# Kernel optimization log

Hardware: AMD Instinct MI355X
Metric: run time of the kernel (lower is better)

Reference implementation:

```python
import jax, jax.numpy as jnp
import numpy as np
import math

D = 256   # d_model / hidden_size
Q = 256   # q_num (query-side nodes)
K = 512   # k_num (key-side nodes)
NEG = -9e15


def _forward(q_enc, k_enc, rel_k, rel_v, k_adj,
             W_glob, b_glob, W_gv0, b_gv0, W_gv1, b_gv1,
             W_gq, b_gq, W_lq, b_lq,
             W_locgate, b_locgate, W_gate, b_gate):
    d = q_enc.shape[-1]
    scale = 1.0 / math.sqrt(d)
    act = jnp.tanh  # activation_func='tanh'

    # --- global sigmoid blending of k_enc with the mean query encoding ---
    q_glob_enc = jnp.mean(q_enc, axis=0)                       # [d]
    k_s = jax.nn.sigmoid((q_glob_enc @ W_glob + b_glob) @ k_enc.T * scale)  # [K]
    k_s = k_s[:, None]                                         # [K,1]
    g_1 = q_glob_enc @ W_gv0 + b_gv0                           # [d]
    k_1 = k_enc @ W_gv1 + b_gv1                                # [K,d]
    k_enc2 = (1.0 - k_s) * k_1 + k_s * g_1                     # [K,d]

    # --- global relation-aware attention over k nodes ---
    q_glob = q_enc @ W_gq + b_gq                               # [Q,d]
    qk_logit = q_glob @ k_enc2.T                               # [Q,K]
    qk_r = jnp.einsum('qd,qkd->qk', q_glob, rel_k)             # [Q,K]
    glob_attn = jax.nn.softmax(act((qk_logit + qk_r) * scale), axis=-1)  # [Q,K]

    # --- local adjacency-masked attention ---
    q_loc = q_enc @ W_lq + b_lq                                # [Q,d]
    qnk_logit = q_loc @ k_enc2.T                               # [Q,K]
    qnk_r = jnp.einsum('qd,qkd->qk', q_loc, rel_k)             # [Q,K]
    loc_attn = act((qnk_logit + qnk_r) * scale)                # [Q,K]
    # loc_weight_rep[q,i,j] = loc_attn[q,j]  (repeat + view in torch)
    mask = (k_adj != 0)[None, :, :]                            # [1,K,K]
    masked = jnp.where(mask, loc_attn[:, None, :], NEG)        # [Q,K,K]
    attn_adj_norm = jax.nn.softmax(masked, axis=-1)            # [Q,K,K]
    k_loc = jnp.einsum('qij,jd->qid', attn_adj_norm, k_enc2)   # [Q,K,d]

    # --- local gate between neighborhood value and self value ---
    # sigmoid(cat([k_loc, k_self]) @ W_locgate + b); k_self is broadcast k_enc2
    Wg1, Wg2 = W_locgate[:d], W_locgate[d:]                    # [d,1] each
    gate_logit = (jnp.einsum('qid,d->qi', k_loc, Wg1[:, 0])
                  + (k_enc2 @ Wg2)[None, :, 0] + b_locgate[0])  # [Q,K]
    loc_gate = jax.nn.sigmoid(gate_logit)[..., None]           # [Q,K,1]
    k_awr = loc_gate * k_loc + (1.0 - loc_gate) * k_enc2[None, :, :]  # [Q,K,d]

    # --- aggregate with global attention + relation values ---
    k_matmul = jnp.einsum('qk,qkd->qd', glob_attn, k_awr)      # [Q,d]
    k_r_matmul = jnp.einsum('qk,qkd->qd', glob_attn, rel_v)    # [Q,d]
    q_enc_new = k_matmul + k_r_matmul                          # [Q,d]

    # --- residual gate ---
    Wq1, Wq2 = W_gate[:d], W_gate[d:]
    gate = jax.nn.sigmoid(q_enc_new @ Wq1 + q_enc @ Wq2 + b_gate)  # [Q,1]
    h = gate * q_enc_new + (1.0 - gate) * q_enc                # [Q,d]
    return h


def setup_inputs() -> dict:
    key = jax.random.key(0)
    ks = jax.random.split(key, 16)
    def w(k, shape):
        return jax.random.normal(k, shape, jnp.float32) * 0.02
    return {
        'q_enc': jax.random.normal(ks[0], (Q, D), jnp.float32),
        'k_enc': jax.random.normal(ks[1], (K, D), jnp.float32),
        'rel_k': jax.random.normal(ks[2], (Q, K, D), jnp.float32) * 0.1,
        'rel_v': jax.random.normal(ks[3], (Q, K, D), jnp.float32) * 0.1,
        'k_adj': jax.random.randint(ks[4], (K, K), 0, 2, jnp.int64) if jax.config.jax_enable_x64 else jax.random.randint(ks[4], (K, K), 0, 2, jnp.int32),
        'W_glob': w(ks[5], (D, D)), 'b_glob': jnp.zeros((D,), jnp.float32),
        'W_gv0': w(ks[6], (D, D)), 'b_gv0': jnp.zeros((D,), jnp.float32),
        'W_gv1': w(ks[7], (D, D)), 'b_gv1': jnp.zeros((D,), jnp.float32),
        'W_gq': w(ks[8], (D, D)), 'b_gq': jnp.zeros((D,), jnp.float32),
        'W_lq': w(ks[9], (D, D)), 'b_lq': jnp.zeros((D,), jnp.float32),
        'W_locgate': w(ks[10], (2 * D, 1)), 'b_locgate': jnp.zeros((1,), jnp.float32),
        'W_gate': w(ks[11], (2 * D, 1)), 'b_gate': jnp.zeros((1,), jnp.float32),
    }


def reference(q_enc, k_enc, rel_k, rel_v, k_adj,
              W_glob, b_glob, W_gv0, b_gv0, W_gv1, b_gv1,
              W_gq, b_gq, W_lq, b_lq,
              W_locgate, b_locgate, W_gate, b_gate):
    return _forward(q_enc, k_enc, rel_k, rel_v, k_adj,
                    W_glob, b_glob, W_gv0, b_gv0, W_gv1, b_gv1,
                    W_gq, b_gq, W_lq, b_lq,
                    W_locgate, b_locgate, W_gate, b_gate)
```

## Files before the change

kernel.cpp:

```cpp
#include <hip/hip_runtime.h>
#include <math.h>

#define QN 256
#define KN 512
#define DN 256
#define SCALE 0.0625f

typedef __attribute__((ext_vector_type(8))) short short8v;
typedef __attribute__((ext_vector_type(4))) float f32x4;

__device__ __forceinline__ float sigf(float x){ return 1.0f/(1.0f+expf(-x)); }

__device__ __forceinline__ unsigned short f2bf(float x){
  unsigned u = __float_as_uint(x);
  unsigned r = (u + 0x7FFFu + ((u >> 16) & 1u)) >> 16;
  return (unsigned short)r;
}

__device__ __forceinline__ short8v ld8(const unsigned short* p){
  ushort4 a = *(const ushort4*)p;
  ushort4 b = *(const ushort4*)(p + 16);
  short8v r;
  r[0]=(short)a.x; r[1]=(short)a.y; r[2]=(short)a.z; r[3]=(short)a.w;
  r[4]=(short)b.x; r[5]=(short)b.y; r[6]=(short)b.z; r[7]=(short)b.w;
  return r;
}

__device__ __forceinline__ float wave_red(float v){
  #pragma unroll
  for (int off = 32; off; off >>= 1) v += __shfl_down(v, off);
  return v;
}

__global__ void kA2(const float* __restrict__ q_enc,
                    const float* __restrict__ W_glob, const float* __restrict__ W_gv0,
                    float* __restrict__ party0, float* __restrict__ party1,
                    const int* __restrict__ kadj, unsigned short* __restrict__ mbf){
  __shared__ float sm[256][9];
  __shared__ float qm[8];
  int b = blockIdx.x, t = threadIdx.x;
  int j0 = b*8;
  #pragma unroll
  for (int i = 0; i < 8; ++i){
    int gi = b*2048 + i*256 + t;
    int4 v = ((const int4*)kadj)[gi];
    ushort4 o;
    o.x = v.x ? 0x3F80 : 0; o.y = v.y ? 0x3F80 : 0;
    o.z = v.z ? 0x3F80 : 0; o.w = v.w ? 0x3F80 : 0;
    ((ushort4*)mbf)[gi] = o;
  }
  float4 lo = *(const float4*)(q_enc + (size_t)t*DN + j0);
  float4 hi = *(const float4*)(q_enc + (size_t)t*DN + j0 + 4);
  sm[t][0]=lo.x; sm[t][1]=lo.y; sm[t][2]=lo.z; sm[t][3]=lo.w;
  sm[t][4]=hi.x; sm[t][5]=hi.y; sm[t][6]=hi.z; sm[t][7]=hi.w;
  __syncthreads();
  #pragma unroll
  for (int s = 128; s > 0; s >>= 1){
    if (t < s){
      #pragma unroll
      for (int j = 0; j < 8; ++j) sm[t][j] += sm[t+s][j];
    }
    __syncthreads();
  }
  if (t < 8) qm[t] = sm[0][t] * (1.0f/QN);
  __syncthreads();
  float a0 = 0.f, a1 = 0.f;
  #pragma unroll
  for (int j = 0; j < 8; ++j){
    float s = qm[j];
    a0 = fmaf(s, W_glob[(size_t)(j0+j)*DN + t], a0);
    a1 = fmaf(s, W_gv0[(size_t)(j0+j)*DN + t], a1);
  }
  party0[b*256 + t] = a0; party1[b*256 + t] = a1;
}

__global__ void k23(const float* __restrict__ k_enc,
                    const float* __restrict__ W_gv1, const float* __restrict__ b_gv1,
                    const float* __restrict__ party0, const float* __restrict__ party1,
                    const float* __restrict__ b_glob, const float* __restrict__ b_gv0,
                    const float* __restrict__ W_locgate,
                    float* __restrict__ k_enc2, float* __restrict__ cvec,
                    float* __restrict__ gl2,
                    const float* __restrict__ q_enc,
                    const float* __restrict__ W_gq, const float* __restrict__ b_gq,
                    const float* __restrict__ W_lq, const float* __restrict__ b_lq,
                    float* __restrict__ q_glob, float* __restrict__ q_loc){
  __shared__ float sh1[256];
  __shared__ float red8[8];
  int bid = blockIdx.x, t = threadIdx.x;
  int w = t >> 6, lane = t & 63;
  if (bid < 512){
    int k = bid;
    float tg = b_glob[t], g1v = b_gv0[t];
    #pragma unroll 8
    for (int b2 = 0; b2 < 32; ++b2){
      tg  += party0[b2*256 + t];
      g1v += party1[b2*256 + t];
    }
    float kv = k_enc[(size_t)k*DN + t];
    sh1[t] = kv;
    float part = wave_red(kv * tg);
    if (lane == 0) red8[w] = part;
    __syncthreads();
    float dot = red8[0] + red8[1] + red8[2] + red8[3];
    float ks = sigf(dot * SCALE);
    float acc = b_gv1[t];
    #pragma unroll 8
    for (int j = 0; j < DN; ++j) acc = fmaf(sh1[j], W_gv1[(size_t)j*DN + t], acc);
    float v = (1.f - ks)*acc + ks*g1v;
    k_enc2[(size_t)k*DN + t] = v;
    float pc = wave_red(v * W_locgate[t]);
    float pg = wave_red(v * W_locgate[DN + t]);
    __syncthreads();
    if (lane == 0){ red8[w] = pc; red8[4 + w] = pg; }
    __syncthreads();
    if (t == 0) cvec[k] = red8[0] + red8[1] + red8[2] + red8[3];
    if (t == 1) gl2[k]  = red8[4] + red8[5] + red8[6] + red8[7];
  } else {
    int q = bid - 512;
    sh1[t] = q_enc[(size_t)q*DN + t];
    __syncthreads();
    float a = b_gq[t], b = b_lq[t];
    #pragma unroll 8
    for (int j = 0; j < DN; ++j){
      float s = sh1[j];
      a = fmaf(s, W_gq[(size_t)j*DN + t], a);
      b = fmaf(s, W_lq[(size_t)j*DN + t], b);
    }
    q_glob[(size_t)q*DN + t] = a; q_loc[(size_t)q*DN + t] = b;
  }
}

__global__ __launch_bounds__(256) void kbf(const float* __restrict__ rel_k,
                    const float* __restrict__ rel_v,
                    const float* __restrict__ q_glob, const float* __restrict__ q_loc,
                    const float* __restrict__ ke2, const float* __restrict__ cvec,
                    float* __restrict__ exs,
                    unsigned short* __restrict__ ebf, unsigned short* __restrict__ ecbf,
                    float* __restrict__ part){
  __shared__ f32x4 sacc[4][16][4];
  int t = threadIdx.x;
  int wv = t >> 6, lane = t & 63;
  int g = lane >> 4, l16 = lane & 15;
  int b = blockIdx.x;
  int q = b >> 3, slice = b & 7;
  int base = lane & 48;
  float4 a4[4], b4[4];
  #pragma unroll
  for (int it = 0; it < 4; ++it){
    int d = it*64 + l16*4;
    a4[it] = *(const float4*)(q_glob + (size_t)q*DN + d);
    b4[it] = *(const float4*)(q_loc  + (size_t)q*DN + d);
  }
  f32x4 racc[4];
  #pragma unroll
  for (int it = 0; it < 4; ++it) racc[it] = (f32x4){0.f,0.f,0.f,0.f};

  int k = slice*64 + wv*4 + g;
  size_t ro = ((size_t)q*KN + k)*DN;
  f32x4 x[4], y[4];
  #pragma unroll
  for (int it = 0; it < 4; ++it){
    int d = it*64 + l16*4;
    x[it] = __builtin_nontemporal_load((const f32x4*)(rel_k + ro + d));
    y[it] = __builtin_nontemporal_load((const f32x4*)(rel_v + ro + d));
  }
  #pragma unroll
  for (int kq = 0; kq < 4; ++kq){
    f32x4 xn[4], yn[4];
    if (kq < 3){
      size_t ro2 = ((size_t)q*KN + (k + 16))*DN;
      #pragma unroll
      for (int it = 0; it < 4; ++it){
        int d = it*64 + l16*4;
        xn[it] = __builtin_nontemporal_load((const f32x4*)(rel_k + ro2 + d));
        yn[it] = __builtin_nontemporal_load((const f32x4*)(rel_v + ro2 + d));
      }
    }
    float p1 = 0.f, p2 = 0.f, p3 = 0.f, p4 = 0.f;
    #pragma unroll
    for (int it = 0; it < 4; ++it){
      int d = it*64 + l16*4;
      float4 c = *(const float4*)(ke2 + (size_t)k*DN + d);
      float4 a = a4[it], bb = b4[it];
      p1 += x[it][0]*a.x  + x[it][1]*a.y  + x[it][2]*a.z  + x[it][3]*a.w;
      p2 += x[it][0]*bb.x + x[it][1]*bb.y + x[it][2]*bb.z + x[it][3]*bb.w;
      p3 += c.x*a.x  + c.y*a.y  + c.z*a.z  + c.w*a.w;
      p4 += c.x*bb.x + c.y*bb.y + c.z*bb.z + c.w*bb.w;
    }
    #pragma unroll
    for (int off = 8; off; off >>= 1){
      p1 += __shfl_down(p1, off); p2 += __shfl_down(p2, off);
      p3 += __shfl_down(p3, off); p4 += __shfl_down(p4, off);
    }
    float p13 = __shfl(p1 + p3, base);
    float p24 = __shfl(p2 + p4, base);
    float exv = expf(tanhf(p13*SCALE));
    float evv = expf(tanhf(p24*SCALE));
    if (l16 == 0){
      size_t idx = (size_t)q*KN + k;
      exs[idx] = exv;
      ebf[idx] = f2bf(evv);
      ecbf[idx] = f2bf(evv * cvec[k]);
    }
    #pragma unroll
    for (int it = 0; it < 4; ++it){
      racc[it][0] = fmaf(exv, y[it][0], racc[it][0]);
      racc[it][1] = fmaf(exv, y[it][1], racc[it][1]);
      racc[it][2] = fmaf(exv, y[it][2], racc[it][2]);
      racc[it][3] = fmaf(exv, y[it][3], racc[it][3]);
    }
    if (kq < 3){
      #pragma unroll
      for (int it = 0; it < 4; ++it){ x[it] = xn[it]; y[it] = yn[it]; }
      k += 16;
    }
  }
  #pragma unroll
  for (int h = 16; h <= 32; h <<= 1){
    #pragma unroll
    for (int it = 0; it < 4; ++it){
      racc[it][0] += __shfl_xor(racc[it][0], h);
      racc[it][1] += __shfl_xor(racc[it][1], h);
      racc[it][2] += __shfl_xor(racc[it][2], h);
      racc[it][3] += __shfl_xor(racc[it][3], h);
    }
  }
  if (lane < 16){
    #pragma unroll
    for (int it = 0; it < 4; ++it) sacc[wv][lane][it] = racc[it];
  }
  __syncthreads();
  if (t < 64){
    int it = t >> 4, lb = t & 15;
    f32x4 r0 = sacc[0][lb][it], r1 = sacc[1][lb][it];
    f32x4 r2 = sacc[2][lb][it], r3 = sacc[3][lb][it];
    f32x4 r = r0 + r1 + r2 + r3;
    int d = it*64 + lb*4;
    *(f32x4*)(part + ((size_t)slice*QN + q)*DN + d) = r;
  }
}

__global__ __launch_bounds__(256) void kcA2m(const unsigned short* __restrict__ ebf,
                                             const unsigned short* __restrict__ ecbf,
                                             const unsigned short* __restrict__ mbf,
                                             const float* __restrict__ exs,
                                             const float* __restrict__ gl2,
                                             const float* __restrict__ blg_p,
                                             unsigned short* __restrict__ wvbf,
                                             float* __restrict__ v2){
  __shared__ unsigned short Ae[16*520];
  __shared__ unsigned short Ac[16*520];
  __shared__ unsigned short Bm[64*520];
  int t = threadIdx.x;
  int i0 = blockIdx.x*64, q0 = blockIdx.y*16;
  #pragma unroll
  for (int it = 0; it < 4; ++it){
    int c = t + 256*it; int row = c >> 6, col = (c & 63)*8;
    *(uint4*)&Ae[row*520 + col] = *(const uint4*)&ebf[(size_t)(q0+row)*KN + col];
    *(uint4*)&Ac[row*520 + col] = *(const uint4*)&ecbf[(size_t)(q0+row)*KN + col];
  }
  #pragma unroll
  for (int it = 0; it < 16; ++it){
    int c = t + 256*it; int row = c >> 6, col = (c & 63)*8;
    *(uint4*)&Bm[row*520 + col] = *(const uint4*)&mbf[(size_t)(i0+row)*KN + col];
  }
  __syncthreads();
  int w = t >> 6, l = t & 63;
  int g16 = l >> 4, l16 = l & 15;
  f32x4 aS = {0.f,0.f,0.f,0.f}, aN = {0.f,0.f,0.f,0.f};
  const unsigned short* pe = &Ae[l16*520];
  const unsigned short* pc = &Ac[l16*520];
  const unsigned short* pb = &Bm[(16*w + l16)*520];
  #pragma unroll
  for (int kk = 0; kk < 16; ++kk){
    int k0 = kk*32 + 4*g16;
    short8v fa = ld8(pe + k0);
    short8v fc = ld8(pc + k0);
    short8v fb = ld8(pb + k0);
    aS = __builtin_amdgcn_mfma_f32_16x16x32_bf16(fa, fb, aS, 0, 0, 0);
    aN = __builtin_amdgcn_mfma_f32_16x16x32_bf16(fc, fb, aN, 0, 0, 0);
  }
  float blg = blg_p[0];
  int i = i0 + 16*w + l16;
  float gli = gl2[i];
  #pragma unroll
  for (int r = 0; r < 4; ++r){
    int q = q0 + 4*g16 + r;
    size_t idx = (size_t)q*KN + i;
    float s = aS[r], n = aN[r];
    float lgv = sigf(n/s + gli + blg);
    float ex = exs[idx];
    wvbf[idx] = f2bf(ex*lgv/s);
    v2[idx] = ex*(1.f - lgv);
  }
}

__global__ __launch_bounds__(256) void kcC2m(const unsigned short* __restrict__ wvbf,
                                             const unsigned short* __restrict__ mbf,
                                             const unsigned short* __restrict__ ebf,
                                             const float* __restrict__ v2,
                                             float* __restrict__ coef){
  __shared__ unsigned short Aw[16*520];
  __shared__ unsigned short Bm2[512*72];
  int t = threadIdx.x;
  int j0 = blockIdx.x*64, q0 = blockIdx.y*16;
  #pragma unroll
  for (int it = 0; it < 4; ++it){
    int c = t + 256*it; int row = c >> 6, col = (c & 63)*8;
    *(uint4*)&Aw[row*520 + col] = *(const uint4*)&wvbf[(size_t)(q0+row)*KN + col];
  }
  #pragma unroll
  for (int it = 0; it < 16; ++it){
    int c = t + 256*it; int row = c >> 3, col = (c & 7)*8;
    *(uint4*)&Bm2[row*72 + col] = *(const uint4*)&mbf[(size_t)row*KN + j0 + col];
  }
  __syncthreads();
  int w = t >> 6, l = t & 63;
  int g16 = l >> 4, l16 = l & 15;
  f32x4 aU = {0.f,0.f,0.f,0.f};
  const unsigned short* pa = &Aw[l16*520];
  int nn = 16*w + l16;
  #pragma unroll
  for (int kk = 0; kk < 16; ++kk){
    int k0 = kk*32 + 4*g16;
    short8v fa = ld8(pa + k0);
    short8v fb;
    #pragma unroll
    for (int e = 0; e < 4; ++e){
      fb[e]   = (short)Bm2[(k0+e)*72 + nn];
      fb[4+e] = (short)Bm2[(k0+16+e)*72 + nn];
    }
    aU = __builtin_amdgcn_mfma_f32_16x16x32_bf16(fa, fb, aU, 0, 0, 0);
  }
  int j = j0 + nn;
  #pragma unroll
  for (int r = 0; r < 4; ++r){
    int q = q0 + 4*g16 + r;
    size_t idx = (size_t)q*KN + j;
    float evv = __uint_as_float(((unsigned)ebf[idx]) << 16);
    coef[idx] = aU[r]*evv + v2[idx];
  }
}

__global__ __launch_bounds__(1024) void kE2(const float* __restrict__ ke2,
                                            const float* __restrict__ exs,
                                            const float* __restrict__ coef,
                                            const float* __restrict__ part,
                                            const float* __restrict__ q_enc,
                                            const float* __restrict__ W_gate,
                                            const float* __restrict__ b_gate,
                                            float* __restrict__ out){
  __shared__ float red[512];
  __shared__ float4 pacc[16][64];
  int q = blockIdx.x, t = threadIdx.x, w = t >> 6, lane = t & 63;
  if (t < 512) red[t] = exs[(size_t)q*KN + t];
  __syncthreads();
  #pragma unroll
  for (int s = 256; s > 0; s >>= 1){
    if (t < s) red[t] += red[t+s];
    __syncthreads();
  }
  float invs = 1.0f / red[0];
  float4 acc;
  if ((w & 1) == 0){
    f32x4 pv = *(const f32x4*)(part + ((size_t)(w >> 1)*QN + q)*DN + lane*4);
    acc = make_float4(pv[0], pv[1], pv[2], pv[3]);
  } else {
    acc = make_float4(0.f, 0.f, 0.f, 0.f);
  }
  int kbase = w*32;
  #pragma unroll 8
  for (int kk = 0; kk < 32; ++kk){
    int k = kbase + kk;
    float ck = coef[(size_t)q*KN + k];
    float4 kv = ((const float4*)(ke2 + (size_t)k*DN))[lane];
    acc.x = fmaf(ck, kv.x, acc.x);
    acc.y = fmaf(ck, kv.y, acc.y);
    acc.z = fmaf(ck, kv.z, acc.z);
    acc.w = fmaf(ck, kv.w, acc.w);
  }
  pacc[w][lane] = acc;
  __syncthreads();
  if (t < 64){
    float4 r = pacc[0][t];
    #pragma unroll
    for (int w2 = 1; w2 < 16; ++w2){
      float4 p = pacc[w2][t];
      r.x += p.x; r.y += p.y; r.z += p.z; r.w += p.w;
    }
    r.x *= invs; r.y *= invs; r.z *= invs; r.w *= invs;
    float4 qe = ((const float4*)(q_enc + (size_t)q*DN))[t];
    float4 w1 = ((const float4*)(W_gate))[t];
    float4 w2v = ((const float4*)(W_gate + DN))[t];
    float pd = r.x*w1.x + r.y*w1.y + r.z*w1.z + r.w*w1.w
             + qe.x*w2v.x + qe.y*w2v.y + qe.z*w2v.z + qe.w*w2v.w;
    #pragma unroll
    for (int off = 32; off; off >>= 1) pd += __shfl_down(pd, off);
    float gate = sigf(__shfl(pd, 0) + b_gate[0]);
    float4 h;
    h.x = gate*r.x + (1.f-gate)*qe.x;
    h.y = gate*r.y + (1.f-gate)*qe.y;
    h.z = gate*r.z + (1.f-gate)*qe.z;
    h.w = gate*r.w + (1.f-gate)*qe.w;
    ((float4*)(out + (size_t)q*DN))[t] = h;
  }
}

extern "C" void kernel_launch(void* const* d_in, const int* in_sizes, int n_in,
                              void* d_out, int out_size, void* d_ws, size_t ws_size,
                              hipStream_t stream){
  const float* q_enc     = (const float*)d_in[0];
  const float* k_enc     = (const float*)d_in[1];
  const float* rel_k     = (const float*)d_in[2];
  const float* rel_v     = (const float*)d_in[3];
  const int*   k_adj     = (const int*)  d_in[4];
  const float* W_glob    = (const float*)d_in[5];
  const float* b_glob    = (const float*)d_in[6];
  const float* W_gv0     = (const float*)d_in[7];
  const float* b_gv0     = (const float*)d_in[8];
  const float* W_gv1     = (const float*)d_in[9];
  const float* b_gv1     = (const float*)d_in[10];
  const float* W_gq      = (const float*)d_in[11];
  const float* b_gq      = (const float*)d_in[12];
  const float* W_lq      = (const float*)d_in[13];
  const float* b_lq      = (const float*)d_in[14];
  const float* W_locgate = (const float*)d_in[15];
  const float* b_locgate = (const float*)d_in[16];
  const float* W_gate    = (const float*)d_in[17];
  const float* b_gate    = (const float*)d_in[18];
  float* out = (float*)d_out;

  float* ws = (float*)d_ws;
  float* party0   = ws;
  float* party1   = party0 + 8192;
  float* k_enc2   = party1 + 8192;
  float* cvec     = k_enc2 + 131072;
  float* gl2      = cvec + 512;
  float* q_glob   = gl2 + 512;
  float* q_loc    = q_glob + 65536;
  float* exs      = q_loc + 65536;
  float* v2       = exs + 131072;
  float* coef     = v2 + 131072;
  float* part     = coef + 131072;
  unsigned short* mbf  = (unsigned short*)(part + 524288);
  unsigned short* ebf  = mbf + 262144;
  unsigned short* ecbf = ebf + 131072;
  unsigned short* wvbf = ecbf + 131072;

  kA2<<<32, 256, 0, stream>>>(q_enc, W_glob, W_gv0, party0, party1, k_adj, mbf);
  k23<<<768, 256, 0, stream>>>(k_enc, W_gv1, b_gv1, party0, party1, b_glob, b_gv0,
                               W_locgate, k_enc2, cvec, gl2,
                               q_enc, W_gq, b_gq, W_lq, b_lq, q_glob, q_loc);
  kbf<<<2048, 256, 0, stream>>>(rel_k, rel_v, q_glob, q_loc, k_enc2, cvec,
                                exs, ebf, ecbf, part);
  kcA2m<<<dim3(8, 16), 256, 0, stream>>>(ebf, ecbf, mbf, exs, gl2, b_locgate, wvbf, v2);
  kcC2m<<<dim3(8, 16), 256, 0, stream>>>(wvbf, mbf, ebf, v2, coef);
  kE2<<<256, 1024, 0, stream>>>(k_enc2, exs, coef, part, q_enc, W_gate, b_gate, out);
}
```

Baseline: 88.41 us.

## Fuse masked-coefficient matmul kernel into final output kernel

Removes the separate MFMA kernel that computed coef = (wv @ mask) * e + v2 and folds it into the final per-query kernel. The fused version computes it with scalar FMAs reading the bf16 adjacency matrix directly, and keeps the coefficients in shared memory. This saves one launch and the coef round trip through global memory. In exchange, each of the 256 blocks rereads the full 512x512 bf16 mask (about 512KB per block, mostly from L2) and does the work on scalar ALUs instead of matrix cores.

```diff
diff --git a/kernel.cpp b/kernel.cpp
--- a/kernel.cpp
+++ b/kernel.cpp
@@ -296,65 +296,27 @@
   }
 }
 
-__global__ __launch_bounds__(256) void kcC2m(const unsigned short* __restrict__ wvbf,
-                                             const unsigned short* __restrict__ mbf,
-                                             const unsigned short* __restrict__ ebf,
-                                             const float* __restrict__ v2,
-                                             float* __restrict__ coef){
-  __shared__ unsigned short Aw[16*520];
-  __shared__ unsigned short Bm2[512*72];
-  int t = threadIdx.x;
-  int j0 = blockIdx.x*64, q0 = blockIdx.y*16;
-  #pragma unroll
-  for (int it = 0; it < 4; ++it){
-    int c = t + 256*it; int row = c >> 6, col = (c & 63)*8;
-    *(uint4*)&Aw[row*520 + col] = *(const uint4*)&wvbf[(size_t)(q0+row)*KN + col];
-  }
-  #pragma unroll
-  for (int it = 0; it < 16; ++it){
-    int c = t + 256*it; int row = c >> 3, col = (c & 7)*8;
-    *(uint4*)&Bm2[row*72 + col] = *(const uint4*)&mbf[(size_t)row*KN + j0 + col];
-  }
-  __syncthreads();
-  int w = t >> 6, l = t & 63;
-  int g16 = l >> 4, l16 = l & 15;
-  f32x4 aU = {0.f,0.f,0.f,0.f};
-  const unsigned short* pa = &Aw[l16*520];
-  int nn = 16*w + l16;
-  #pragma unroll
-  for (int kk = 0; kk < 16; ++kk){
-    int k0 = kk*32 + 4*g16;
-    short8v fa = ld8(pa + k0);
-    short8v fb;
-    #pragma unroll
-    for (int e = 0; e < 4; ++e){
-      fb[e]   = (short)Bm2[(k0+e)*72 + nn];
-      fb[4+e] = (short)Bm2[(k0+16+e)*72 + nn];
-    }
-    aU = __builtin_amdgcn_mfma_f32_16x16x32_bf16(fa, fb, aU, 0, 0, 0);
-  }
-  int j = j0 + nn;
-  #pragma unroll
-  for (int r = 0; r < 4; ++r){
-    int q = q0 + 4*g16 + r;
-    size_t idx = (size_t)q*KN + j;
-    float evv = __uint_as_float(((unsigned)ebf[idx]) << 16);
-    coef[idx] = aU[r]*evv + v2[idx];
-  }
-}
-
-__global__ __launch_bounds__(1024) void kE2(const float* __restrict__ ke2,
+__global__ __launch_bounds__(1024) void kE3(const float* __restrict__ ke2,
                                             const float* __restrict__ exs,
-                                            const float* __restrict__ coef,
+                                            const unsigned short* __restrict__ wvbf,
+                                            const unsigned short* __restrict__ mbf,
+                                            const unsigned short* __restrict__ ebf,
+                                            const float* __restrict__ v2,
                                             const float* __restrict__ part,
                                             const float* __restrict__ q_enc,
                                             const float* __restrict__ W_gate,
                                             const float* __restrict__ b_gate,
                                             float* __restrict__ out){
   __shared__ float red[512];
+  __shared__ float wvs[512];
+  __shared__ float sacc[4][512];
+  __shared__ float coefs[512];
   __shared__ float4 pacc[16][64];
   int q = blockIdx.x, t = threadIdx.x, w = t >> 6, lane = t & 63;
-  if (t < 512) red[t] = exs[(size_t)q*KN + t];
+  if (t < 512){
+    red[t] = exs[(size_t)q*KN + t];
+    wvs[t] = __uint_as_float(((unsigned)wvbf[(size_t)q*KN + t]) << 16);
+  }
   __syncthreads();
   #pragma unroll
   for (int s = 256; s > 0; s >>= 1){
@@ -362,6 +324,28 @@
     __syncthreads();
   }
   float invs = 1.0f / red[0];
+  {
+    int tq = t & 255, ti = t >> 8;
+    int j0 = tq*2;
+    float a0 = 0.f, a1 = 0.f;
+    int ibase = ti*128;
+    #pragma unroll 8
+    for (int ii = 0; ii < 128; ++ii){
+      int i = ibase + ii;
+      unsigned mm = *(const unsigned*)(mbf + (size_t)i*KN + j0);
+      float wvi = wvs[i];
+      a0 = fmaf(wvi, __uint_as_float((mm & 0xFFFFu) << 16), a0);
+      a1 = fmaf(wvi, __uint_as_float((mm >> 16) << 16), a1);
+    }
+    sacc[ti][j0] = a0; sacc[ti][j0+1] = a1;
+  }
+  __syncthreads();
+  if (t < 512){
+    float u = sacc[0][t] + sacc[1][t] + sacc[2][t] + sacc[3][t];
+    float evv = __uint_as_float(((unsigned)ebf[(size_t)q*KN + t]) << 16);
+    coefs[t] = u*evv + v2[(size_t)q*KN + t];
+  }
+  __syncthreads();
   float4 acc;
   if ((w & 1) == 0){
     f32x4 pv = *(const f32x4*)(part + ((size_t)(w >> 1)*QN + q)*DN + lane*4);
@@ -373,7 +357,7 @@
   #pragma unroll 8
   for (int kk = 0; kk < 32; ++kk){
     int k = kbase + kk;
-    float ck = coef[(size_t)q*KN + k];
+    float ck = coefs[k];
     float4 kv = ((const float4*)(ke2 + (size_t)k*DN))[lane];
     acc.x = fmaf(ck, kv.x, acc.x);
     acc.y = fmaf(ck, kv.y, acc.y);
@@ -441,8 +425,7 @@
   float* q_loc    = q_glob + 65536;
   float* exs      = q_loc + 65536;
   float* v2       = exs + 131072;
-  float* coef     = v2 + 131072;
-  float* part     = coef + 131072;
+  float* part     = v2 + 131072;
   unsigned short* mbf  = (unsigned short*)(part + 524288);
   unsigned short* ebf  = mbf + 262144;
   unsigned short* ecbf = ebf + 131072;
@@ -455,6 +438,6 @@
   kbf<<<2048, 256, 0, stream>>>(rel_k, rel_v, q_glob, q_loc, k_enc2, cvec,
                                 exs, ebf, ecbf, part);
   kcA2m<<<dim3(8, 16), 256, 0, stream>>>(ebf, ecbf, mbf, exs, gl2, b_locgate, wvbf, v2);
-  kcC2m<<<dim3(8, 16), 256, 0, stream>>>(wvbf, mbf, ebf, v2, coef);
-  kE2<<<256, 1024, 0, stream>>>(k_enc2, exs, coef, part, q_enc, W_gate, b_gate, out);
-}
+  kE3<<<256, 1024, 0, stream>>>(k_enc2, exs, wvbf, mbf, ebf, v2, part,
+                                q_enc, W_gate, b_gate, out);
+}
```

Measured after the change: 89.58 us. Within noise of the previous version (+1.3%).
